# Kernel optimization log

Measured on AMD Instinct MI355X. Metric: run time of the kernel, lower is better.

The kernel has to match this reference:

```python
import jax, jax.numpy as jnp
import numpy as np

TEMP = 0.5  # matches temperature init kwarg
EPS = 1e-12  # F.normalize eps


def _l2norm(x):
    # F.normalize(x, dim=1): x / max(||x||, eps)
    n = jnp.linalg.norm(x, axis=1, keepdims=True)
    return x / jnp.maximum(n, EPS)


def setup_inputs() -> dict:
    key = jax.random.key(0)
    k1, k2 = jax.random.split(key)
    B, D = 4096, 256
    return {
        "x_i": jax.random.normal(k1, (B, D), dtype=jnp.float32),
        "x_j": jax.random.normal(k2, (B, D), dtype=jnp.float32),
    }


def reference(x_i, x_j):
    B = x_i.shape[0]
    z = jnp.concatenate([_l2norm(x_i), _l2norm(x_j)], axis=0)  # [2B, D]
    # cosine similarity of normalized rows == matmul (avoids NxNxD broadcast)
    sim = (z @ z.T) / TEMP  # [2B, 2B]
    idx = jnp.arange(B)
    # diagonals at offsets +B and -B = positive pairs
    pos = jnp.concatenate([sim[idx, idx + B], sim[idx + B, idx]])  # [2B]
    exp_sim = jnp.exp(sim)
    # neg = all off-diagonal entries per row (neg_mask = ~eye(2B))
    exp_neg = exp_sim.sum(axis=1) - jnp.exp(jnp.diagonal(sim))  # [2B]
    exp_pos = jnp.exp(pos)
    loss = -jnp.log(exp_pos / (exp_pos + exp_neg))
    return loss.mean()
```

## Files before the change

### kernel.cpp

```cpp
#include <hip/hip_runtime.h>
#include <hip/hip_bf16.h>

typedef __attribute__((ext_vector_type(8))) int   i32x8;
typedef __attribute__((ext_vector_type(4))) int   i32x4;
typedef __attribute__((ext_vector_type(4))) float f32x4;

constexpr int BB = 4096;
constexpr int D  = 256;
constexpr int R2 = 8192;
constexpr int NSPLIT = 32;
constexpr int CPB = R2 / NSPLIT;
constexpr int NG  = CPB / 16;
constexpr float SCALE = 1.6986436005760381f;
constexpr float E2 = 7.38905609893065f;

__device__ __forceinline__ void async16(const unsigned char* g, unsigned char* l) {
    __builtin_amdgcn_global_load_lds(
        (const __attribute__((address_space(1))) void*)g,
        (__attribute__((address_space(3))) void*)l,
        16, 0, 0);
}

#define MFMA8(A, B, C) \
    __builtin_amdgcn_mfma_scale_f32_16x16x128_f8f6f4((A), (B), (C), 0, 0, 0, 127, 0, 127)

__global__ __launch_bounds__(256) void norm_kernel(const float* __restrict__ xi,
                                                   const float* __restrict__ xj,
                                                   int* __restrict__ z8,
                                                   float* __restrict__ pos,
                                                   float* __restrict__ out) {
    const int wid = threadIdx.x >> 6, lane = threadIdx.x & 63;
    const int k = blockIdx.x * 4 + wid;
    if (blockIdx.x == 0 && threadIdx.x == 0) out[0] = 0.f;
    const float4* a4 = reinterpret_cast<const float4*>(xi + (size_t)k * D);
    const float4* b4 = reinterpret_cast<const float4*>(xj + (size_t)k * D);
    float4 a = a4[lane], b = b4[lane];
    float ssi = a.x*a.x + a.y*a.y + a.z*a.z + a.w*a.w;
    float ssj = b.x*b.x + b.y*b.y + b.z*b.z + b.w*b.w;
    float dot = a.x*b.x + a.y*b.y + a.z*b.z + a.w*b.w;
#pragma unroll
    for (int off = 32; off; off >>= 1) {
        ssi += __shfl_xor(ssi, off);
        ssj += __shfl_xor(ssj, off);
        dot += __shfl_xor(dot, off);
    }
    const float inv_i = 1.0f / fmaxf(sqrtf(ssi), 1e-12f);
    const float inv_j = 1.0f / fmaxf(sqrtf(ssj), 1e-12f);
    const float si = inv_i * SCALE, sj = inv_j * SCALE;
    int pi = __builtin_amdgcn_cvt_pk_fp8_f32(a.x*si, a.y*si, 0, false);
    pi     = __builtin_amdgcn_cvt_pk_fp8_f32(a.z*si, a.w*si, pi, true);
    int pj = __builtin_amdgcn_cvt_pk_fp8_f32(b.x*sj, b.y*sj, 0, false);
    pj     = __builtin_amdgcn_cvt_pk_fp8_f32(b.z*sj, b.w*sj, pj, true);
    z8[(size_t)k * 64 + lane]        = pi;
    z8[(size_t)(k + BB) * 64 + lane] = pj;
    if (lane == 0) pos[k] = dot * inv_i * inv_j * 2.0f;
}

__global__ __launch_bounds__(256) void sim_kernel(const unsigned char* __restrict__ z8,
                                                  float* __restrict__ partial) {
    __shared__ unsigned char tb[CPB * D];
    const int tid = threadIdx.x;
    const int wid = tid >> 6, lane = tid & 63;
    const int lrow = lane & 15, quad = lane >> 4;
    const int r0 = blockIdx.x * 256 + wid * 64;
    const int cbase = blockIdx.y * CPB;

    {
        const int srow16 = tid >> 4;
        const int srcg   = (tid & 15) ^ srow16;
        const unsigned char* gs = z8 + (size_t)(cbase + srow16) * D + srcg * 16;
        unsigned char* ds = tb + tid * 16;
#pragma unroll
        for (int i = 0; i < 16; ++i)
            async16(gs + (size_t)i * 16 * D, ds + i * 4096);
    }

    const unsigned char* abase = z8 + (size_t)(r0 + lrow) * D + quad * 32;
    i32x8 a0k0 = *reinterpret_cast<const i32x8*>(abase             );
    i32x8 a0k1 = *reinterpret_cast<const i32x8*>(abase        + 128);
    i32x8 a1k0 = *reinterpret_cast<const i32x8*>(abase + 16*D      );
    i32x8 a1k1 = *reinterpret_cast<const i32x8*>(abase + 16*D + 128);
    i32x8 a2k0 = *reinterpret_cast<const i32x8*>(abase + 32*D      );
    i32x8 a2k1 = *reinterpret_cast<const i32x8*>(abase + 32*D + 128);
    i32x8 a3k0 = *reinterpret_cast<const i32x8*>(abase + 48*D      );
    i32x8 a3k1 = *reinterpret_cast<const i32x8*>(abase + 48*D + 128);
    asm volatile("" : "+v"(a0k0), "+v"(a0k1), "+v"(a1k0), "+v"(a1k1),
                      "+v"(a2k0), "+v"(a2k1), "+v"(a3k0), "+v"(a3k1));

    f32x4 racc0 = {0.f,0.f,0.f,0.f}, racc1 = {0.f,0.f,0.f,0.f};
    f32x4 racc2 = {0.f,0.f,0.f,0.f}, racc3 = {0.f,0.f,0.f,0.f};

    __syncthreads();

    const int pe0 = (quad * 2) ^ lrow;
    const int pe1 = (8 + quad * 2) ^ lrow;
    const unsigned char* rbp = tb + lrow * D;
#pragma unroll 4
    for (int n = 0; n < NG; ++n) {
        const i32x4 lo0 = *reinterpret_cast<const i32x4*>(rbp + pe0*16);
        const i32x4 hi0 = *reinterpret_cast<const i32x4*>(rbp + (pe0^1)*16);
        const i32x4 lo1 = *reinterpret_cast<const i32x4*>(rbp + pe1*16);
        const i32x4 hi1 = *reinterpret_cast<const i32x4*>(rbp + (pe1^1)*16);
        rbp += 16 * D;
        const i32x8 b0 = __builtin_shufflevector(lo0, hi0, 0,1,2,3,4,5,6,7);
        const i32x8 b1 = __builtin_shufflevector(lo1, hi1, 0,1,2,3,4,5,6,7);

        f32x4 c0 = {0.f,0.f,0.f,0.f}, c1 = {0.f,0.f,0.f,0.f};
        f32x4 c2 = {0.f,0.f,0.f,0.f}, c3 = {0.f,0.f,0.f,0.f};
        c0 = MFMA8(a0k0, b0, c0);  c0 = MFMA8(a0k1, b1, c0);
        c1 = MFMA8(a1k0, b0, c1);  c1 = MFMA8(a1k1, b1, c1);
        c2 = MFMA8(a2k0, b0, c2);  c2 = MFMA8(a2k1, b1, c2);
        c3 = MFMA8(a3k0, b0, c3);  c3 = MFMA8(a3k1, b1, c3);

        racc0[0] += __builtin_amdgcn_exp2f(c0[0]);
        racc0[1] += __builtin_amdgcn_exp2f(c0[1]);
        racc0[2] += __builtin_amdgcn_exp2f(c0[2]);
        racc0[3] += __builtin_amdgcn_exp2f(c0[3]);
        racc1[0] += __builtin_amdgcn_exp2f(c1[0]);
        racc1[1] += __builtin_amdgcn_exp2f(c1[1]);
        racc1[2] += __builtin_amdgcn_exp2f(c1[2]);
        racc1[3] += __builtin_amdgcn_exp2f(c1[3]);
        racc2[0] += __builtin_amdgcn_exp2f(c2[0]);
        racc2[1] += __builtin_amdgcn_exp2f(c2[1]);
        racc2[2] += __builtin_amdgcn_exp2f(c2[2]);
        racc2[3] += __builtin_amdgcn_exp2f(c2[3]);
        racc3[0] += __builtin_amdgcn_exp2f(c3[0]);
        racc3[1] += __builtin_amdgcn_exp2f(c3[1]);
        racc3[2] += __builtin_amdgcn_exp2f(c3[2]);
        racc3[3] += __builtin_amdgcn_exp2f(c3[3]);
    }

#define REDUCE_STORE(RV, M)                                                     \
    {                                                                           \
        _Pragma("unroll")                                                       \
        for (int j = 0; j < 4; ++j) {                                           \
            float v = (RV)[j];                                                  \
            v += __shfl_xor(v, 1);                                              \
            v += __shfl_xor(v, 2);                                              \
            v += __shfl_xor(v, 4);                                              \
            v += __shfl_xor(v, 8);                                              \
            if (lrow == 0)                                                      \
                partial[(size_t)blockIdx.y * R2 + r0 + (M)*16 + quad*4 + j] = v;\
        }                                                                       \
    }
    REDUCE_STORE(racc0, 0)
    REDUCE_STORE(racc1, 1)
    REDUCE_STORE(racc2, 2)
    REDUCE_STORE(racc3, 3)
#undef REDUCE_STORE
}

__global__ __launch_bounds__(256) void reduce_kernel(const float* __restrict__ partial,
                                                     const float* __restrict__ pos,
                                                     float* __restrict__ out) {
    __shared__ float wsum[4];
    const int tid = threadIdx.x;
    const int r = blockIdx.x * 256 + tid;
    float S = 0.f;
#pragma unroll
    for (int s = 0; s < NSPLIT; ++s) S += partial[(size_t)s * R2 + r];
    const float p = pos[r & (BB - 1)];
    float lsum = __logf(__expf(p) + S - E2) - p;
#pragma unroll
    for (int off = 32; off; off >>= 1) lsum += __shfl_xor(lsum, off);
    if ((tid & 63) == 0) wsum[tid >> 6] = lsum;
    __syncthreads();
    if (tid == 0) {
        float t = wsum[0] + wsum[1] + wsum[2] + wsum[3];
        atomicAdd(out, t * (1.0f / (float)R2));
    }
}

extern "C" void kernel_launch(void* const* d_in, const int* in_sizes, int n_in,
                              void* d_out, int out_size, void* d_ws, size_t ws_size,
                              hipStream_t stream) {
    (void)in_sizes; (void)n_in; (void)out_size; (void)ws_size;
    const float* xi = (const float*)d_in[0];
    const float* xj = (const float*)d_in[1];
    float* out = (float*)d_out;

    unsigned char* z8 = (unsigned char*)d_ws;
    float* partial = (float*)((char*)d_ws + (size_t)R2 * D);
    float* pos     = (float*)((char*)d_ws + (size_t)R2 * D + (size_t)NSPLIT*R2*4);

    norm_kernel<<<BB / 4, 256, 0, stream>>>(xi, xj, (int*)z8, pos, out);
    sim_kernel<<<dim3(R2 / 256, NSPLIT), 256, 0, stream>>>(z8, partial);
    reduce_kernel<<<R2 / 256, 256, 0, stream>>>(partial, pos, out);
}
```

Measured before the change: 87.96 us.

## Exploit similarity symmetry: compute upper-triangle tiles and scatter column sums atomically

Uses the symmetry of z·zᵀ so that only upper-triangular 256x256 tiles are computed. Each off-diagonal tile adds its exponentiated values to both the row sums and the column sums through float atomics. This roughly halves the MFMA and exp work and removes the per-split partial buffer and its reduction loop. In exchange, half the launched blocks exit immediately, which leaves load imbalance, and atomic contention plus nondeterministic summation order are introduced.

Measured after the change: 104.9 us. +19.3%, slower.

```diff
diff --git a/kernel.cpp b/kernel.cpp
--- a/kernel.cpp
+++ b/kernel.cpp
@@ -8,9 +8,8 @@
 constexpr int BB = 4096;
 constexpr int D  = 256;
 constexpr int R2 = 8192;
-constexpr int NSPLIT = 32;
-constexpr int CPB = R2 / NSPLIT;
-constexpr int NG  = CPB / 16;
+constexpr int TB = 256;
+constexpr int NG = TB / 16;
 constexpr float SCALE = 1.6986436005760381f;
 constexpr float E2 = 7.38905609893065f;
 
@@ -28,10 +27,12 @@
                                                    const float* __restrict__ xj,
                                                    int* __restrict__ z8,
                                                    float* __restrict__ pos,
+                                                   float* __restrict__ S,
                                                    float* __restrict__ out) {
     const int wid = threadIdx.x >> 6, lane = threadIdx.x & 63;
     const int k = blockIdx.x * 4 + wid;
     if (blockIdx.x == 0 && threadIdx.x == 0) out[0] = 0.f;
+    if (blockIdx.x < 32) S[blockIdx.x * 256 + threadIdx.x] = 0.f;
     const float4* a4 = reinterpret_cast<const float4*>(xi + (size_t)k * D);
     const float4* b4 = reinterpret_cast<const float4*>(xj + (size_t)k * D);
     float4 a = a4[lane], b = b4[lane];
@@ -57,13 +58,16 @@
 }
 
 __global__ __launch_bounds__(256) void sim_kernel(const unsigned char* __restrict__ z8,
-                                                  float* __restrict__ partial) {
-    __shared__ unsigned char tb[CPB * D];
+                                                  float* __restrict__ S) {
+    const int bi = blockIdx.x, bj = blockIdx.y;
+    if (bj < bi) return;
+    __shared__ unsigned char tb[TB * D];
     const int tid = threadIdx.x;
     const int wid = tid >> 6, lane = tid & 63;
     const int lrow = lane & 15, quad = lane >> 4;
-    const int r0 = blockIdx.x * 256 + wid * 64;
-    const int cbase = blockIdx.y * CPB;
+    const int r0 = bi * TB + wid * 64;
+    const int cbase = bj * TB;
+    const bool offdiag = (bj != bi);
 
     {
         const int srow16 = tid >> 4;
@@ -89,13 +93,16 @@
 
     f32x4 racc0 = {0.f,0.f,0.f,0.f}, racc1 = {0.f,0.f,0.f,0.f};
     f32x4 racc2 = {0.f,0.f,0.f,0.f}, racc3 = {0.f,0.f,0.f,0.f};
+    float cacc[NG];
+#pragma unroll
+    for (int n = 0; n < NG; ++n) cacc[n] = 0.f;
 
     __syncthreads();
 
     const int pe0 = (quad * 2) ^ lrow;
     const int pe1 = (8 + quad * 2) ^ lrow;
     const unsigned char* rbp = tb + lrow * D;
-#pragma unroll 4
+#pragma unroll
     for (int n = 0; n < NG; ++n) {
         const i32x4 lo0 = *reinterpret_cast<const i32x4*>(rbp + pe0*16);
         const i32x4 hi0 = *reinterpret_cast<const i32x4*>(rbp + (pe0^1)*16);
@@ -112,25 +119,28 @@
         c2 = MFMA8(a2k0, b0, c2);  c2 = MFMA8(a2k1, b1, c2);
         c3 = MFMA8(a3k0, b0, c3);  c3 = MFMA8(a3k1, b1, c3);
 
-        racc0[0] += __builtin_amdgcn_exp2f(c0[0]);
-        racc0[1] += __builtin_amdgcn_exp2f(c0[1]);
-        racc0[2] += __builtin_amdgcn_exp2f(c0[2]);
-        racc0[3] += __builtin_amdgcn_exp2f(c0[3]);
-        racc1[0] += __builtin_amdgcn_exp2f(c1[0]);
-        racc1[1] += __builtin_amdgcn_exp2f(c1[1]);
-        racc1[2] += __builtin_amdgcn_exp2f(c1[2]);
-        racc1[3] += __builtin_amdgcn_exp2f(c1[3]);
-        racc2[0] += __builtin_amdgcn_exp2f(c2[0]);
-        racc2[1] += __builtin_amdgcn_exp2f(c2[1]);
-        racc2[2] += __builtin_amdgcn_exp2f(c2[2]);
-        racc2[3] += __builtin_amdgcn_exp2f(c2[3]);
-        racc3[0] += __builtin_amdgcn_exp2f(c3[0]);
-        racc3[1] += __builtin_amdgcn_exp2f(c3[1]);
-        racc3[2] += __builtin_amdgcn_exp2f(c3[2]);
-        racc3[3] += __builtin_amdgcn_exp2f(c3[3]);
-    }
-
-#define REDUCE_STORE(RV, M)                                                     \
+        const float e00=__builtin_amdgcn_exp2f(c0[0]), e01=__builtin_amdgcn_exp2f(c0[1]);
+        const float e02=__builtin_amdgcn_exp2f(c0[2]), e03=__builtin_amdgcn_exp2f(c0[3]);
+        const float e10=__builtin_amdgcn_exp2f(c1[0]), e11=__builtin_amdgcn_exp2f(c1[1]);
+        const float e12=__builtin_amdgcn_exp2f(c1[2]), e13=__builtin_amdgcn_exp2f(c1[3]);
+        const float e20=__builtin_amdgcn_exp2f(c2[0]), e21=__builtin_amdgcn_exp2f(c2[1]);
+        const float e22=__builtin_amdgcn_exp2f(c2[2]), e23=__builtin_amdgcn_exp2f(c2[3]);
+        const float e30=__builtin_amdgcn_exp2f(c3[0]), e31=__builtin_amdgcn_exp2f(c3[1]);
+        const float e32=__builtin_amdgcn_exp2f(c3[2]), e33=__builtin_amdgcn_exp2f(c3[3]);
+
+        racc0[0]+=e00; racc0[1]+=e01; racc0[2]+=e02; racc0[3]+=e03;
+        racc1[0]+=e10; racc1[1]+=e11; racc1[2]+=e12; racc1[3]+=e13;
+        racc2[0]+=e20; racc2[1]+=e21; racc2[2]+=e22; racc2[3]+=e23;
+        racc3[0]+=e30; racc3[1]+=e31; racc3[2]+=e32; racc3[3]+=e33;
+
+        float cp = ((e00+e01)+(e02+e03)) + ((e10+e11)+(e12+e13))
+                 + ((e20+e21)+(e22+e23)) + ((e30+e31)+(e32+e33));
+        cp += __shfl_xor(cp, 16);
+        cp += __shfl_xor(cp, 32);
+        cacc[n] = cp;
+    }
+
+#define REDUCE_ATOMIC(RV, M)                                                    \
     {                                                                           \
         _Pragma("unroll")                                                       \
         for (int j = 0; j < 4; ++j) {                                           \
@@ -139,28 +149,30 @@
             v += __shfl_xor(v, 2);                                              \
             v += __shfl_xor(v, 4);                                              \
             v += __shfl_xor(v, 8);                                              \
-            if (lrow == 0)                                                      \
-                partial[(size_t)blockIdx.y * R2 + r0 + (M)*16 + quad*4 + j] = v;\
+            if (lrow == 0) atomicAdd(&S[r0 + (M)*16 + quad*4 + j], v);          \
         }                                                                       \
     }
-    REDUCE_STORE(racc0, 0)
-    REDUCE_STORE(racc1, 1)
-    REDUCE_STORE(racc2, 2)
-    REDUCE_STORE(racc3, 3)
-#undef REDUCE_STORE
-}
-
-__global__ __launch_bounds__(256) void reduce_kernel(const float* __restrict__ partial,
+    REDUCE_ATOMIC(racc0, 0)
+    REDUCE_ATOMIC(racc1, 1)
+    REDUCE_ATOMIC(racc2, 2)
+    REDUCE_ATOMIC(racc3, 3)
+#undef REDUCE_ATOMIC
+
+    if (offdiag) {
+#pragma unroll
+        for (int n = 0; n < NG; ++n)
+            if (quad == 0) atomicAdd(&S[cbase + n*16 + lrow], cacc[n]);
+    }
+}
+
+__global__ __launch_bounds__(256) void reduce_kernel(const float* __restrict__ S,
                                                      const float* __restrict__ pos,
                                                      float* __restrict__ out) {
     __shared__ float wsum[4];
     const int tid = threadIdx.x;
     const int r = blockIdx.x * 256 + tid;
-    float S = 0.f;
-#pragma unroll
-    for (int s = 0; s < NSPLIT; ++s) S += partial[(size_t)s * R2 + r];
     const float p = pos[r & (BB - 1)];
-    float lsum = __logf(__expf(p) + S - E2) - p;
+    float lsum = __logf(__expf(p) + S[r] - E2) - p;
 #pragma unroll
     for (int off = 32; off; off >>= 1) lsum += __shfl_xor(lsum, off);
     if ((tid & 63) == 0) wsum[tid >> 6] = lsum;
@@ -180,10 +192,10 @@
     float* out = (float*)d_out;
 
     unsigned char* z8 = (unsigned char*)d_ws;
-    float* partial = (float*)((char*)d_ws + (size_t)R2 * D);
-    float* pos     = (float*)((char*)d_ws + (size_t)R2 * D + (size_t)NSPLIT*R2*4);
-
-    norm_kernel<<<BB / 4, 256, 0, stream>>>(xi, xj, (int*)z8, pos, out);
-    sim_kernel<<<dim3(R2 / 256, NSPLIT), 256, 0, stream>>>(z8, partial);
-    reduce_kernel<<<R2 / 256, 256, 0, stream>>>(partial, pos, out);
-}
+    float* S   = (float*)((char*)d_ws + (size_t)R2 * D);
+    float* pos = (float*)((char*)d_ws + (size_t)R2 * D + R2 * 4);
+
+    norm_kernel<<<BB / 4, 256, 0, stream>>>(xi, xj, (int*)z8, pos, S, out);
+    sim_kernel<<<dim3(R2 / TB, R2 / TB), 256, 0, stream>>>(z8, S);
+    reduce_kernel<<<R2 / 256, 256, 0, stream>>>(S, pos, out);
+}
```
